# Kernel optimization log

Measured on AMD Instinct MI355X. Metric: run time of the kernel, lower is better.

The kernel has to match this reference:

```python
import jax, jax.numpy as jnp
import numpy as np

DIMS = 1024
BATCH, SEQ = 4, 2048

def setup_inputs() -> dict:
    key = jax.random.key(0)
    k1, k2, k3, k4 = jax.random.split(key, 4)
    scale = 1.0 / np.sqrt(DIMS)
    return {
        "input_seq_embs": jax.random.normal(k1, (BATCH, SEQ, DIMS), dtype=jnp.float32),
        "Wq": jax.random.normal(k2, (DIMS, DIMS), dtype=jnp.float32) * scale,
        "Wk": jax.random.normal(k3, (DIMS, DIMS), dtype=jnp.float32) * scale,
        "Wv": jax.random.normal(k4, (DIMS, DIMS), dtype=jnp.float32) * scale,
    }

def reference(input_seq_embs, Wq, Wk, Wv):
    # nn.Linear(x) = x @ W.T ; weights stored [out, in]
    q = jnp.einsum('bsd,ed->bse', input_seq_embs, Wq)
    k = jnp.einsum('bsd,ed->bse', input_seq_embs, Wk)
    v = jnp.einsum('bsd,ed->bse', input_seq_embs, Wv)
    # full N x N scores, NO 1/sqrt(d) scaling (faithful to source)
    scores = jnp.einsum('bqe,bke->bqk', q, k)
    causal = jnp.tril(jnp.ones((q.shape[1], q.shape[1]), dtype=bool))
    scores = jnp.where(causal[None, :, :], scores, -jnp.inf)
    attn = jax.nn.softmax(scores, axis=-1)
    return jnp.einsum('bqk,bke->bqe', attn, v)
```

## Files before the change

### kernel.cpp

```cpp
#include <hip/hip_runtime.h>


typedef _Float16 h8 __attribute__((ext_vector_type(8)));
typedef float f32x4 __attribute__((ext_vector_type(4)));

#define BM 128
#define BN 128

__device__ __forceinline__ void gl_lds16(const _Float16* g, _Float16* l) {
    __builtin_amdgcn_global_load_lds(
        (const __attribute__((address_space(1))) void*)g,
        (__attribute__((address_space(3))) void*)l, 16, 0, 0);
}

template<int SWZ, int OM, bool KLIM>
__global__ __launch_bounds__(256) void gemm_nt(
    const _Float16* __restrict__ A, const _Float16* __restrict__ B,
    void* __restrict__ Cp, int N, int K,
    size_t sAz, size_t sBz, size_t sCz)
{
    __shared__ __align__(16) char smem[32768];
    _Float16* As = (_Float16*)smem;
    _Float16* Bs = (_Float16*)(smem + 16384);

    int bx, by;
    if (SWZ == 1) {
        const int r = blockIdx.x & 7, q2 = blockIdx.x >> 3;
        bx = q2 >> 3;
        by = ((q2 & 7) << 3) | r;
    } else if (SWZ == 2) {
        const int r = blockIdx.x & 7, g = blockIdx.x >> 3;
        if (g <= r) { by = r;      bx = g; }
        else        { by = 15 - r; bx = g - (r + 1); }
    } else {
        const int r = blockIdx.x & 7, g = blockIdx.x >> 3;
        by = (g & 1) ? (15 - r) : r;
        bx = g >> 1;
    }

    const int tid  = threadIdx.x;
    const int lane = tid & 63;
    const int wv   = tid >> 6;
    const int m0 = by * BM, n0 = bx * BN;
    const size_t z = blockIdx.z;

    const int lr = lane >> 2;
    const int lc = (lane & 3) * 8;
    const _Float16* pA0 = A + z * sAz + (size_t)(m0 + wv * 16 + lr) * K + lc;
    const _Float16* pA1 = pA0 + (size_t)64 * K;
    const _Float16* pB0 = B + z * sBz + (size_t)(n0 + wv * 16 + lr) * K + lc;
    const _Float16* pB1 = pB0 + (size_t)64 * K;
    _Float16* lA0 = As + wv * 512;
    _Float16* lA1 = As + (wv + 4) * 512;
    _Float16* lB0 = Bs + wv * 512;
    _Float16* lB1 = Bs + (wv + 4) * 512;

    const int la = lane & 15;
    const int qd = lane >> 4;
    const int wm = (wv >> 1) * 64;
    const int wn = (wv & 1) * 64;

    f32x4 acc[4][4];
    #pragma unroll
    for (int i = 0; i < 4; i++)
        #pragma unroll
        for (int j = 0; j < 4; j++)
            acc[i][j] = (f32x4){0.f, 0.f, 0.f, 0.f};

    const int kEnd = KLIM ? (m0 + BM) : K;

    for (int k0 = 0; k0 < kEnd; k0 += 64) {
        gl_lds16(pA0,      lA0);
        gl_lds16(pA1,      lA1);
        gl_lds16(pB0,      lB0);
        gl_lds16(pB1,      lB1);
        gl_lds16(pA0 + 32, lA0 + 4096);
        gl_lds16(pA1 + 32, lA1 + 4096);
        gl_lds16(pB0 + 32, lB0 + 4096);
        gl_lds16(pB1 + 32, lB1 + 4096);
        pA0 += 64; pA1 += 64; pB0 += 64; pB1 += 64;
        __syncthreads();

        #pragma unroll
        for (int s = 0; s < 2; s++) {
            h8 af[4], bf[4];
            #pragma unroll
            for (int i = 0; i < 4; i++)
                af[i] = *(const h8*)&As[s * 4096 + (wm + i * 16 + la) * 32 + qd * 8];
            #pragma unroll
            for (int i = 0; i < 4; i++)
                bf[i] = *(const h8*)&Bs[s * 4096 + (wn + i * 16 + la) * 32 + qd * 8];
            #pragma unroll
            for (int i = 0; i < 4; i++)
                #pragma unroll
                for (int j = 0; j < 4; j++)
                    acc[i][j] = __builtin_amdgcn_mfma_f32_16x16x32_f16(af[i], bf[j], acc[i][j], 0, 0, 0);
        }
        __syncthreads();
    }

    if (OM == 2) {
        _Float16* C = (_Float16*)Cp;
        #pragma unroll
        for (int i = 0; i < 4; i++)
            #pragma unroll
            for (int j = 0; j < 4; j++) {
                const int col  = n0 + wn + j * 16 + la;
                const size_t base = (size_t)(col >> 10) * 8388608 + (col & 1023);
                #pragma unroll
                for (int rr = 0; rr < 4; rr++)
                    C[base + (size_t)(m0 + wm + i * 16 + qd * 4 + rr) * 1024] =
                        (_Float16)acc[i][j][rr];
            }
    } else {
        float* C = (float*)Cp + z * sCz;
        #pragma unroll
        for (int i = 0; i < 4; i++)
            #pragma unroll
            for (int j = 0; j < 4; j++)
                #pragma unroll
                for (int rr = 0; rr < 4; rr++)
                    C[(size_t)(m0 + wm + i * 16 + qd * 4 + rr) * N + (n0 + wn + j * 16 + la)] =
                        acc[i][j][rr];
    }
}

__global__ __launch_bounds__(256) void cvt_all(
    const float* __restrict__ x, const float* __restrict__ Wq,
    const float* __restrict__ Wk, const float* __restrict__ Wv,
    _Float16* __restrict__ x_h, _Float16* __restrict__ Wh)
{
    const int bid = blockIdx.x;
    const float* src; _Float16* dst; size_t off;
    if (bid < 4096) {
        src = x; dst = x_h; off = (size_t)bid * 2048;
    } else {
        const int b2 = bid - 4096;
        const int w = b2 >> 9;
        src = (w == 0) ? Wq : ((w == 1) ? Wk : Wv);
        dst = Wh + (size_t)w * 1048576;
        off = (size_t)(b2 & 511) * 2048;
    }
    const size_t i = off + (size_t)threadIdx.x * 8;
    float4 a = *(const float4*)(src + i);
    float4 b = *(const float4*)(src + i + 4);
    h8 o = { (_Float16)a.x, (_Float16)a.y, (_Float16)a.z, (_Float16)a.w,
             (_Float16)b.x, (_Float16)b.y, (_Float16)b.z, (_Float16)b.w };
    *(h8*)(dst + i) = o;
}

__global__ __launch_bounds__(256) void softmax_causal(const float* __restrict__ S,
                                                      _Float16* __restrict__ P)
{
    const int idx = blockIdx.x;
    const int q = idx & 2047;
    const float* Srow = S + (size_t)idx * 2048;
    _Float16* Prow = P + (size_t)idx * 2048;
    const int t = threadIdx.x;
    const int k0 = t * 8;
    const int lane = t & 63, wv = t >> 6;
    __shared__ float red[4];

    float v[8];
    const bool any = (k0 <= q);
    if (any) {
        float4 a = *(const float4*)(Srow + k0);
        float4 b = *(const float4*)(Srow + k0 + 4);
        v[0] = a.x; v[1] = a.y; v[2] = a.z; v[3] = a.w;
        v[4] = b.x; v[5] = b.y; v[6] = b.z; v[7] = b.w;
    }
    float mx = -3.4e38f;
    #pragma unroll
    for (int j = 0; j < 8; j++)
        if (any && k0 + j <= q) mx = fmaxf(mx, v[j]);
    #pragma unroll
    for (int o = 32; o > 0; o >>= 1) mx = fmaxf(mx, __shfl_down(mx, o, 64));
    if (lane == 0) red[wv] = mx;
    __syncthreads();
    const float mall = fmaxf(fmaxf(red[0], red[1]), fmaxf(red[2], red[3]));
    __syncthreads();

    float sum = 0.f;
    #pragma unroll
    for (int j = 0; j < 8; j++) {
        float e = (any && k0 + j <= q) ? __expf(v[j] - mall) : 0.f;
        v[j] = e;
        sum += e;
    }
    #pragma unroll
    for (int o = 32; o > 0; o >>= 1) sum += __shfl_down(sum, o, 64);
    if (lane == 0) red[wv] = sum;
    __syncthreads();
    const float inv = 1.f / (red[0] + red[1] + red[2] + red[3]);

    const int kceil = ((q >> 7) + 1) << 7;
    if (k0 < kceil) {
        h8 o = { (_Float16)(v[0] * inv), (_Float16)(v[1] * inv),
                 (_Float16)(v[2] * inv), (_Float16)(v[3] * inv),
                 (_Float16)(v[4] * inv), (_Float16)(v[5] * inv),
                 (_Float16)(v[6] * inv), (_Float16)(v[7] * inv) };
        *(h8*)(Prow + k0) = o;
    }
}

__global__ __launch_bounds__(256) void transpose_v_kernel(const _Float16* __restrict__ V,
                                                          _Float16* __restrict__ Vt)
{
    __shared__ _Float16 tile[64][72];
    const int b = blockIdx.z;
    const int s0 = blockIdx.x * 64;
    const int e0 = blockIdx.y * 64;
    const _Float16* Vb = V + (size_t)b * 2048 * 1024;
    _Float16* Vtb = Vt + (size_t)b * 1024 * 2048;
    const int r = threadIdx.x >> 2;
    const int c = (threadIdx.x & 3) * 16;

    const _Float16* src = &Vb[(size_t)(s0 + r) * 1024 + e0 + c];
    *(uint4*)&tile[r][c]     = *(const uint4*)src;
    *(uint4*)&tile[r][c + 8] = *(const uint4*)(src + 8);
    __syncthreads();

    h8 o0, o1;
    #pragma unroll
    for (int j = 0; j < 8; j++) o0[j] = tile[c + j][r];
    #pragma unroll
    for (int j = 0; j < 8; j++) o1[j] = tile[c + 8 + j][r];
    _Float16* dst = &Vtb[(size_t)(e0 + r) * 2048 + s0 + c];
    *(h8*)dst       = o0;
    *(h8*)(dst + 8) = o1;
}

extern "C" void kernel_launch(void* const* d_in, const int* in_sizes, int n_in,
                              void* d_out, int out_size, void* d_ws, size_t ws_size,
                              hipStream_t stream) {
    const float* x  = (const float*)d_in[0];
    const float* Wq = (const float*)d_in[1];
    const float* Wk = (const float*)d_in[2];
    const float* Wv = (const float*)d_in[3];
    float* out = (float*)d_out;

    const size_t MiB = 1024 * 1024;
    char* ws = (char*)d_ws;
    _Float16* QKVh = (_Float16*)ws;
    _Float16* Vh   = QKVh + (size_t)2 * 8388608;
    float*    S    = (float*)(ws + 48 * MiB);
    _Float16* x_h  = (_Float16*)(ws + 48 * MiB);
    _Float16* Wh   = (_Float16*)(ws + 64 * MiB);
    _Float16* P    = (_Float16*)ws;
    _Float16* Vt   = (_Float16*)(ws + 48 * MiB);

    const dim3 blk(256);

    cvt_all<<<dim3(5632), blk, 0, stream>>>(x, Wq, Wk, Wv, x_h, Wh);

    gemm_nt<1, 2, false><<<dim3(1536), blk, 0, stream>>>(
        x_h, Wh, QKVh, 3072, 1024, 0, 0, 0);

    gemm_nt<2, 0, false><<<dim3(136, 1, 4), blk, 0, stream>>>(
        QKVh, QKVh + 8388608, S, 2048, 1024,
        (size_t)2097152, (size_t)2097152, (size_t)4194304);

    softmax_causal<<<dim3(4 * 2048), blk, 0, stream>>>(S, P);

    transpose_v_kernel<<<dim3(32, 16, 4), blk, 0, stream>>>(Vh, Vt);

    gemm_nt<3, 0, true><<<dim3(128, 1, 4), blk, 0, stream>>>(
        P, Vt, out, 1024, 2048,
        (size_t)4194304, (size_t)2097152, (size_t)2097152);
}
```

Measured before the change: 256.3 us.

## Fuse V transpose into QKV GEMM epilogue and swizzle LDS layout

The QKV projection GEMM now writes the V part directly in transposed [b][e][s] layout through its epilogue, so the separate transpose kernel and its extra read and write of V are gone. Vt is placed in the V slot of the QKV buffer. Separately, the LDS tile layout gets an XOR swizzle applied consistently on the global-to-LDS load offsets and the fragment reads, to reduce LDS bank conflicts in every GEMM. The transposed epilogue does strided 8-byte stores, which may coalesce poorly.

```diff
diff --git a/kernel.cpp b/kernel.cpp
--- a/kernel.cpp
+++ b/kernel.cpp
@@ -2,6 +2,7 @@
 
 
 typedef _Float16 h8 __attribute__((ext_vector_type(8)));
+typedef _Float16 h4 __attribute__((ext_vector_type(4)));
 typedef float f32x4 __attribute__((ext_vector_type(4)));
 
 #define BM 128
@@ -45,7 +46,7 @@
     const size_t z = blockIdx.z;
 
     const int lr = lane >> 2;
-    const int lc = (lane & 3) * 8;
+    const int lc = ((lane & 3) ^ ((lane >> 3) & 3)) * 8;
     const _Float16* pA0 = A + z * sAz + (size_t)(m0 + wv * 16 + lr) * K + lc;
     const _Float16* pA1 = pA0 + (size_t)64 * K;
     const _Float16* pB0 = B + z * sBz + (size_t)(n0 + wv * 16 + lr) * K + lc;
@@ -59,6 +60,7 @@
     const int qd = lane >> 4;
     const int wm = (wv >> 1) * 64;
     const int wn = (wv & 1) * 64;
+    const int sg = (qd ^ ((la >> 1) & 3)) * 8;
 
     f32x4 acc[4][4];
     #pragma unroll
@@ -86,10 +88,10 @@
             h8 af[4], bf[4];
             #pragma unroll
             for (int i = 0; i < 4; i++)
-                af[i] = *(const h8*)&As[s * 4096 + (wm + i * 16 + la) * 32 + qd * 8];
-            #pragma unroll
-            for (int i = 0; i < 4; i++)
-                bf[i] = *(const h8*)&Bs[s * 4096 + (wn + i * 16 + la) * 32 + qd * 8];
+                af[i] = *(const h8*)&As[s * 4096 + (wm + i * 16 + la) * 32 + sg];
+            #pragma unroll
+            for (int i = 0; i < 4; i++)
+                bf[i] = *(const h8*)&Bs[s * 4096 + (wn + i * 16 + la) * 32 + sg];
             #pragma unroll
             for (int i = 0; i < 4; i++)
                 #pragma unroll
@@ -101,17 +103,35 @@
 
     if (OM == 2) {
         _Float16* C = (_Float16*)Cp;
-        #pragma unroll
-        for (int i = 0; i < 4; i++)
-            #pragma unroll
-            for (int j = 0; j < 4; j++) {
-                const int col  = n0 + wn + j * 16 + la;
-                const size_t base = (size_t)(col >> 10) * 8388608 + (col & 1023);
-                #pragma unroll
-                for (int rr = 0; rr < 4; rr++)
-                    C[base + (size_t)(m0 + wm + i * 16 + qd * 4 + rr) * 1024] =
-                        (_Float16)acc[i][j][rr];
+        if (n0 < 2048) {
+            #pragma unroll
+            for (int i = 0; i < 4; i++)
+                #pragma unroll
+                for (int j = 0; j < 4; j++) {
+                    const int col  = n0 + wn + j * 16 + la;
+                    const size_t base = (size_t)(col >> 10) * 8388608 + (col & 1023);
+                    #pragma unroll
+                    for (int rr = 0; rr < 4; rr++)
+                        C[base + (size_t)(m0 + wm + i * 16 + qd * 4 + rr) * 1024] =
+                            (_Float16)acc[i][j][rr];
+                }
+        } else {
+            _Float16* Vt = C + (size_t)2 * 8388608;
+            #pragma unroll
+            for (int i = 0; i < 4; i++) {
+                const int m  = m0 + wm + i * 16 + qd * 4;
+                const int b  = m >> 11;
+                const int sl = m & 2047;
+                _Float16* Vb = Vt + (size_t)b * 2097152 + sl;
+                #pragma unroll
+                for (int j = 0; j < 4; j++) {
+                    const int e = n0 - 2048 + wn + j * 16 + la;
+                    h4 vv = { (_Float16)acc[i][j][0], (_Float16)acc[i][j][1],
+                              (_Float16)acc[i][j][2], (_Float16)acc[i][j][3] };
+                    *(h4*)(Vb + (size_t)e * 2048) = vv;
+                }
             }
+        }
     } else {
         float* C = (float*)Cp + z * sCz;
         #pragma unroll
@@ -203,33 +223,6 @@
     }
 }
 
-__global__ __launch_bounds__(256) void transpose_v_kernel(const _Float16* __restrict__ V,
-                                                          _Float16* __restrict__ Vt)
-{
-    __shared__ _Float16 tile[64][72];
-    const int b = blockIdx.z;
-    const int s0 = blockIdx.x * 64;
-    const int e0 = blockIdx.y * 64;
-    const _Float16* Vb = V + (size_t)b * 2048 * 1024;
-    _Float16* Vtb = Vt + (size_t)b * 1024 * 2048;
-    const int r = threadIdx.x >> 2;
-    const int c = (threadIdx.x & 3) * 16;
-
-    const _Float16* src = &Vb[(size_t)(s0 + r) * 1024 + e0 + c];
-    *(uint4*)&tile[r][c]     = *(const uint4*)src;
-    *(uint4*)&tile[r][c + 8] = *(const uint4*)(src + 8);
-    __syncthreads();
-
-    h8 o0, o1;
-    #pragma unroll
-    for (int j = 0; j < 8; j++) o0[j] = tile[c + j][r];
-    #pragma unroll
-    for (int j = 0; j < 8; j++) o1[j] = tile[c + 8 + j][r];
-    _Float16* dst = &Vtb[(size_t)(e0 + r) * 2048 + s0 + c];
-    *(h8*)dst       = o0;
-    *(h8*)(dst + 8) = o1;
-}
-
 extern "C" void kernel_launch(void* const* d_in, const int* in_sizes, int n_in,
                               void* d_out, int out_size, void* d_ws, size_t ws_size,
                               hipStream_t stream) {
@@ -242,12 +235,11 @@
     const size_t MiB = 1024 * 1024;
     char* ws = (char*)d_ws;
     _Float16* QKVh = (_Float16*)ws;
-    _Float16* Vh   = QKVh + (size_t)2 * 8388608;
+    _Float16* Vt   = QKVh + (size_t)2 * 8388608;
     float*    S    = (float*)(ws + 48 * MiB);
     _Float16* x_h  = (_Float16*)(ws + 48 * MiB);
     _Float16* Wh   = (_Float16*)(ws + 64 * MiB);
     _Float16* P    = (_Float16*)ws;
-    _Float16* Vt   = (_Float16*)(ws + 48 * MiB);
 
     const dim3 blk(256);
 
@@ -262,8 +254,6 @@
 
     softmax_causal<<<dim3(4 * 2048), blk, 0, stream>>>(S, P);
 
-    transpose_v_kernel<<<dim3(32, 16, 4), blk, 0, stream>>>(Vh, Vt);
-
     gemm_nt<3, 0, true><<<dim3(128, 1, 4), blk, 0, stream>>>(
         P, Vt, out, 1024, 2048,
         (size_t)4194304, (size_t)2097152, (size_t)2097152);
```

Result: faster. 242.0 us (-5.6%).
